# Kernel tuning notes

Measured on AMD Instinct MI355X. Metric: run time of the kernel, lower is better.

## Reference

```python
import jax, jax.numpy as jnp
import numpy as np

GAMMA = 2.0
EPS = 1e-06
LAMBDA_DISTANCE = 1.0
LAMBDA_NORMAL = 0.01
LAMBDA_LAPLACIAN = 0.1
CLS = 1


def vertex_normals(v, f, eps=EPS):
    # v: [N,3], f: [F,3] int. Scatter face normals to vertices, then normalize.
    fv = v[f]  # [F,3,3]
    fn = jnp.cross(fv[:, 1] - fv[:, 0], fv[:, 2] - fv[:, 0])  # [F,3]
    vn = jnp.zeros_like(v)
    vn = vn.at[f[:, 0]].add(fn).at[f[:, 1]].add(fn).at[f[:, 2]].add(fn)
    norm = jnp.maximum(jnp.linalg.norm(vn, axis=-1, keepdims=True), eps)
    return vn / norm


def squared_cdist(a, b):
    # [Na,3] x [Nb,3] -> squared euclidean distances [Na,Nb] (clamped >= 0)
    a2 = jnp.sum(a * a, axis=1)[:, None]
    b2 = jnp.sum(b * b, axis=1)[None, :]
    d2 = a2 + b2 - 2.0 * (a @ b.T)
    return jnp.maximum(d2, 0.0)


def sample_binary_targets(label, v, cls=CLS):
    # Nearest-neighbor grid_sample, align_corners=True, padding zeros.
    # grid = 2*v - 1 -> voxel index = round(v * (size-1)); v[:,0]->W, v[:,1]->H, v[:,2]->D.
    D, H, W = label.shape[2], label.shape[3], label.shape[4]
    ix = jnp.round(v[:, 0] * (W - 1)).astype(jnp.int32)
    iy = jnp.round(v[:, 1] * (H - 1)).astype(jnp.int32)
    iz = jnp.round(v[:, 2] * (D - 1)).astype(jnp.int32)
    inb = (ix >= 0) & (ix < W) & (iy >= 0) & (iy < H) & (iz >= 0) & (iz < D)
    ixc = jnp.clip(ix, 0, W - 1)
    iyc = jnp.clip(iy, 0, H - 1)
    izc = jnp.clip(iz, 0, D - 1)
    vals = (label[0, 0, izc, iyc, ixc] == cls).astype(jnp.float32)
    return jnp.where(inb, vals, 0.0)


def spatial_consistency_loss(rel_pos, targets, gamma=GAMMA, eps=EPS):
    p = jnp.clip(rel_pos, eps, 1.0 - eps)
    pos = targets > 0.5
    pc = jnp.sum(pos).astype(p.dtype)
    tot = jnp.asarray(p.shape[0], p.dtype)
    nc = tot - pc
    alpha = nc / (tot + eps)
    lpos = -alpha * jnp.power(1.0 - p, gamma) * jnp.log(p)
    lneg = -(1.0 - alpha) * jnp.power(p, gamma) * jnp.log(1.0 - p)
    return jnp.sum(jnp.where(pos, lpos, lneg)) / (tot + eps)


def laplacian_uniform(v, f):
    # Uniform mesh Laplacian smoothing: || mean(neighbors) - v ||, averaged.
    i = jnp.concatenate([f[:, 0], f[:, 1], f[:, 2], f[:, 1], f[:, 2], f[:, 0]])
    j = jnp.concatenate([f[:, 1], f[:, 2], f[:, 0], f[:, 0], f[:, 1], f[:, 2]])
    nsum = jnp.zeros_like(v).at[i].add(v[j])
    deg = jnp.zeros((v.shape[0],), v.dtype).at[i].add(1.0)
    lap = nsum / jnp.maximum(deg, 1.0)[:, None] - v
    return jnp.mean(jnp.linalg.norm(lap, axis=1))


def loss_forward(pred_vertices, relative_positions, gt_vertices, pred_faces, gt_faces, label):
    gt_v = jax.lax.stop_gradient(gt_vertices)  # gt comes from label volume; detached in original
    gt_normals = vertex_normals(gt_v, gt_faces)
    # spatial (focal-style) loss
    targets = sample_binary_targets(label, pred_vertices)
    spatial = spatial_consistency_loss(relative_positions, targets)
    # chamfer-style squared surface distance
    d2 = squared_cdist(pred_vertices, gt_v)  # [Np,Ng]
    distance = jnp.mean(jnp.min(d2, axis=1)) + jnp.mean(jnp.min(d2, axis=0))
    # normal consistency vs nearest gt vertex
    pred_normals = vertex_normals(pred_vertices, pred_faces)
    nearest = jnp.argmin(d2, axis=1)
    normal = jnp.mean((pred_normals - gt_normals[nearest]) ** 2)
    # uniform laplacian smoothing
    laplacian = laplacian_uniform(pred_vertices, pred_faces)
    total = spatial + LAMBDA_DISTANCE * distance + LAMBDA_NORMAL * normal + LAMBDA_LAPLACIAN * laplacian
    return total


def setup_inputs() -> dict:
    key = jax.random.key(0)
    k1, k2, k3, k4, k5, k6 = jax.random.split(key, 6)
    Np, Ng = 8192, 12000
    pred_vertices = jax.random.uniform(k1, (Np, 3), dtype=jnp.float32)
    relative_positions = jax.random.uniform(k2, (Np,), dtype=jnp.float32)
    gt_vertices = jax.random.uniform(k3, (Ng, 3), dtype=jnp.float32)
    pred_faces = jax.random.randint(k4, (2 * Np, 3), 0, Np, dtype=jnp.int32)
    gt_faces = jax.random.randint(k5, (2 * Ng, 3), 0, Ng, dtype=jnp.int32)
    label = jax.random.randint(k6, (1, 1, 96, 96, 96), 0, 2, dtype=jnp.int32)
    return {"pred_vertices": pred_vertices, "relative_positions": relative_positions,
            "gt_vertices": gt_vertices, "pred_faces": pred_faces,
            "gt_faces": gt_faces, "label": label}


def reference(pred_vertices, relative_positions, gt_vertices, pred_faces, gt_faces, label):
    return loss_forward(pred_vertices, relative_positions, gt_vertices, pred_faces, gt_faces, label)
```

## Files before the change

kernel.cpp:

```cpp
#include <hip/hip_runtime.h>
#include <math.h>

#define NP 8192
#define NG 12000
#define NFP 16384
#define NFG 24000
#define EPSF 1e-6f

#define GR 16
#define NC (GR*GR*GR)
#define HCELL 0.0625f
#define QL 16
#define QPB (256 / QL)
#define PRED_QBLOCKS (NP / QPB)
#define GT_QBLOCKS (NG / QPB)
#define FACE_BLOCKS ((NFG + NFP + 255) / 256)
#define QF_BLOCKS (PRED_QBLOCKS + GT_QBLOCKS + FACE_BLOCKS)
#define FIN_BLOCKS (NP / 256)

static constexpr size_t OFF_STARTP = 0;
static constexpr size_t OFF_STARTG = 16640;
static constexpr size_t OFF_SORTP  = 33280;
static constexpr size_t OFF_SORTG  = 164352;
static constexpr size_t OFF_GTN    = 356352;
static constexpr size_t OFF_PNN    = 500352;
static constexpr size_t OFF_NSUM   = 598656;
static constexpr size_t OFF_DEG    = 696960;
static constexpr size_t OFF_NEAR   = 729728;
static constexpr size_t OFF_ACCUM  = 762496;
static constexpr size_t OFF_DONE   = 762528;
#define N_ZERO 101545

__device__ __forceinline__ int cell_of(float x) {
    int c = (int)(x * (float)GR);
    return min(max(c, 0), GR - 1);
}

__device__ __forceinline__ void build_cells(const float* __restrict__ pts, int n,
                                            unsigned* __restrict__ start,
                                            float4* __restrict__ sorted,
                                            unsigned* h, unsigned* wsum) {
    int t = threadIdx.x;
    int lane = t & 63, wid = t >> 6;
    for (int i = t; i < NC; i += 1024) h[i] = 0u;
    __syncthreads();
    for (int i = t; i < n; i += 1024) {
        int c = (cell_of(pts[3*i+2]) * GR + cell_of(pts[3*i+1])) * GR + cell_of(pts[3*i]);
        atomicAdd(&h[c], 1u);
    }
    __syncthreads();
    unsigned a0 = h[4*t], a1 = h[4*t+1], a2 = h[4*t+2], a3 = h[4*t+3];
    unsigned tsum = a0 + a1 + a2 + a3;
    unsigned x = tsum;
    #pragma unroll
    for (int off = 1; off < 64; off <<= 1) {
        unsigned y = __shfl_up(x, off, 64);
        if (lane >= off) x += y;
    }
    if (lane == 63) wsum[wid] = x;
    __syncthreads();
    if (t < 16) {
        unsigned w = wsum[t];
        #pragma unroll
        for (int off = 1; off < 16; off <<= 1) {
            unsigned y = __shfl_up(w, off, 64);
            if (t >= off) w += y;
        }
        wsum[t] = w;
    }
    __syncthreads();
    unsigned base = (wid ? wsum[wid-1] : 0u) + (x - tsum);
    unsigned e0 = base, e1 = base + a0, e2 = base + a0 + a1, e3 = base + a0 + a1 + a2;
    start[4*t] = e0; start[4*t+1] = e1; start[4*t+2] = e2; start[4*t+3] = e3;
    h[4*t] = e0; h[4*t+1] = e1; h[4*t+2] = e2; h[4*t+3] = e3;
    __syncthreads();
    for (int i = t; i < n; i += 1024) {
        float px = pts[3*i], py = pts[3*i+1], pz = pts[3*i+2];
        int c = (cell_of(pz) * GR + cell_of(py)) * GR + cell_of(px);
        unsigned pos = atomicAdd(&h[c], 1u);
        sorted[pos] = make_float4(px, py, pz, __int_as_float(i));
    }
    if (t == 0) start[NC] = (unsigned)n;
}

__global__ __launch_bounds__(1024) void build_kernel(const float* __restrict__ pred,
                                                     const float* __restrict__ gt,
                                                     unsigned* __restrict__ startP,
                                                     unsigned* __restrict__ startG,
                                                     float4* __restrict__ sortP,
                                                     float4* __restrict__ sortG,
                                                     float* __restrict__ zero) {
    __shared__ unsigned h[NC];
    __shared__ unsigned wsum[16];
    if (blockIdx.x == 0) {
        build_cells(pred, NP, startP, sortP, h, wsum);
    } else if (blockIdx.x == 1) {
        build_cells(gt, NG, startG, sortG, h, wsum);
    } else {
        int i = (blockIdx.x - 2) * 1024 + threadIdx.x;
        if (i < N_ZERO) zero[i] = 0.0f;
    }
}

__device__ __forceinline__ float wave_sum(float x) {
    #pragma unroll
    for (int o = 32; o > 0; o >>= 1) x += __shfl_down(x, o, 64);
    return x;
}

__device__ __forceinline__ unsigned long long u64min(unsigned long long a,
                                                     unsigned long long b) {
    return a < b ? a : b;
}

__device__ __forceinline__ unsigned long long group_nn(int lane,
                                                       float px, float py, float pz,
                                                       const float4* __restrict__ S,
                                                       const unsigned* __restrict__ cstart) {
    int cx = cell_of(px), cy = cell_of(py), cz = cell_of(pz);
    unsigned long long best = 0xFFFFFFFFFFFFFFFFULL;
    for (int r = 1; ; ++r) {
        int w = 2 * r + 1;
        int nrows = w * w;
        int x0 = max(cx - r, 0), x1 = min(cx + r, GR - 1);
        unsigned long long lb = 0xFFFFFFFFFFFFFFFFULL;
        for (int k = lane; k < nrows; k += QL) {
            int z = cz + k / w - r, y = cy + k % w - r;
            if (z >= 0 && z < GR && y >= 0 && y < GR) {
                int rowbase = (z * GR + y) * GR;
                unsigned s0 = cstart[rowbase + x0];
                unsigned s1 = cstart[rowbase + x1 + 1];
                for (unsigned t = s0; t < s1; ++t) {
                    float4 q = S[t];
                    float ddx = px - q.x, ddy = py - q.y, ddz = pz - q.z;
                    float d2 = fmaf(ddx, ddx, fmaf(ddy, ddy, ddz*ddz));
                    unsigned long long key =
                        ((unsigned long long)__float_as_uint(d2) << 32) |
                        (unsigned)__float_as_int(q.w);
                    lb = u64min(lb, key);
                }
            }
        }
        best = u64min(best, lb);
        #pragma unroll
        for (int m = 1; m < QL; m <<= 1)
            best = u64min(best, (unsigned long long)__shfl_xor((long long)best, m, 64));
        bool covered = (cx - r <= 0) & (cx + r >= GR - 1) &
                       (cy - r <= 0) & (cy + r >= GR - 1) &
                       (cz - r <= 0) & (cz + r >= GR - 1);
        if (covered) break;
        float blo = 1.0e30f;
        if (cx - r > 0)      blo = fminf(blo, px - (float)(cx - r) * HCELL);
        if (cx + r < GR - 1) blo = fminf(blo, (float)(cx + r + 1) * HCELL - px);
        if (cy - r > 0)      blo = fminf(blo, py - (float)(cy - r) * HCELL);
        if (cy + r < GR - 1) blo = fminf(blo, (float)(cy + r + 1) * HCELL - py);
        if (cz - r > 0)      blo = fminf(blo, pz - (float)(cz - r) * HCELL);
        if (cz + r < GR - 1) blo = fminf(blo, (float)(cz + r + 1) * HCELL - pz);
        float bd2 = __uint_as_float((unsigned)(best >> 32));
        if (bd2 <= blo * blo) break;
    }
    return best;
}

__global__ __launch_bounds__(256) void query_face_kernel(const float* __restrict__ pred,
                                                         const int* __restrict__ pf,
                                                         const float* __restrict__ gt,
                                                         const int* __restrict__ gf,
                                                         const float4* __restrict__ sortP,
                                                         const float4* __restrict__ sortG,
                                                         const unsigned* __restrict__ startP,
                                                         const unsigned* __restrict__ startG,
                                                         float* __restrict__ gtn,
                                                         float* __restrict__ pnn,
                                                         float* __restrict__ nsum,
                                                         float* __restrict__ deg,
                                                         int* __restrict__ nearestIdx,
                                                         float* __restrict__ accum) {
    int b = blockIdx.x;
    if (b < PRED_QBLOCKS + GT_QBLOCKS) {
        __shared__ float bs;
        if (threadIdx.x == 0) bs = 0.0f;
        __syncthreads();
        int lane = threadIdx.x & (QL - 1);
        int group = threadIdx.x >> 4;
        float r0 = 0.0f;
        if (b < PRED_QBLOCKS) {
            int qid = b * QPB + group;
            float4 P = sortP[qid];
            unsigned long long key = group_nn(lane, P.x, P.y, P.z, sortG, startG);
            if (lane == 0) {
                int v = __float_as_int(P.w);
                nearestIdx[v] = (int)(unsigned)(key & 0xffffffffu);
                r0 = __uint_as_float((unsigned)(key >> 32));
            }
        } else {
            int qid = (b - PRED_QBLOCKS) * QPB + group;
            float4 Q = sortG[qid];
            unsigned long long key = group_nn(lane, Q.x, Q.y, Q.z, sortP, startP);
            if (lane == 0) r0 = __uint_as_float((unsigned)(key >> 32));
        }
        r0 = wave_sum(r0);
        if ((threadIdx.x & 63) == 0) atomicAdd(&bs, r0);
        __syncthreads();
        if (threadIdx.x == 0)
            atomicAdd(&accum[(b < PRED_QBLOCKS) ? 0 : 6], bs);
    } else {
        int t = (b - PRED_QBLOCKS - GT_QBLOCKS) * 256 + threadIdx.x;
        if (t < NFG) {
            int i0 = gf[3*t], i1 = gf[3*t+1], i2 = gf[3*t+2];
            float ax = gt[3*i0], ay = gt[3*i0+1], az = gt[3*i0+2];
            float bx = gt[3*i1], by = gt[3*i1+1], bz = gt[3*i1+2];
            float cx = gt[3*i2], cy = gt[3*i2+1], cz = gt[3*i2+2];
            float ux = bx-ax, uy = by-ay, uz = bz-az;
            float wx = cx-ax, wy = cy-ay, wz = cz-az;
            float nx = uy*wz - uz*wy, ny = uz*wx - ux*wz, nz = ux*wy - uy*wx;
            atomicAdd(&gtn[3*i0+0], nx); atomicAdd(&gtn[3*i0+1], ny); atomicAdd(&gtn[3*i0+2], nz);
            atomicAdd(&gtn[3*i1+0], nx); atomicAdd(&gtn[3*i1+1], ny); atomicAdd(&gtn[3*i1+2], nz);
            atomicAdd(&gtn[3*i2+0], nx); atomicAdd(&gtn[3*i2+1], ny); atomicAdd(&gtn[3*i2+2], nz);
        } else if (t < NFG + NFP) {
            int u = t - NFG;
            int i0 = pf[3*u], i1 = pf[3*u+1], i2 = pf[3*u+2];
            float ax = pred[3*i0], ay = pred[3*i0+1], az = pred[3*i0+2];
            float bx = pred[3*i1], by = pred[3*i1+1], bz = pred[3*i1+2];
            float cx = pred[3*i2], cy = pred[3*i2+1], cz = pred[3*i2+2];
            float ux = bx-ax, uy = by-ay, uz = bz-az;
            float wx = cx-ax, wy = cy-ay, wz = cz-az;
            float nx = uy*wz - uz*wy, ny = uz*wx - ux*wz, nz = ux*wy - uy*wx;
            atomicAdd(&pnn[3*i0+0], nx); atomicAdd(&pnn[3*i0+1], ny); atomicAdd(&pnn[3*i0+2], nz);
            atomicAdd(&pnn[3*i1+0], nx); atomicAdd(&pnn[3*i1+1], ny); atomicAdd(&pnn[3*i1+2], nz);
            atomicAdd(&pnn[3*i2+0], nx); atomicAdd(&pnn[3*i2+1], ny); atomicAdd(&pnn[3*i2+2], nz);
            atomicAdd(&nsum[3*i0+0], bx+cx); atomicAdd(&nsum[3*i0+1], by+cy); atomicAdd(&nsum[3*i0+2], bz+cz);
            atomicAdd(&nsum[3*i1+0], cx+ax); atomicAdd(&nsum[3*i1+1], cy+ay); atomicAdd(&nsum[3*i1+2], cz+az);
            atomicAdd(&nsum[3*i2+0], ax+bx); atomicAdd(&nsum[3*i2+1], ay+by); atomicAdd(&nsum[3*i2+2], az+bz);
            atomicAdd(&deg[i0], 2.0f); atomicAdd(&deg[i1], 2.0f); atomicAdd(&deg[i2], 2.0f);
        }
    }
}

__global__ __launch_bounds__(256) void finish_kernel(const float* __restrict__ pred,
                                                     const float* __restrict__ relpos,
                                                     const int* __restrict__ label,
                                                     const float* __restrict__ pnn,
                                                     const float* __restrict__ gtn,
                                                     const float* __restrict__ nsum,
                                                     const float* __restrict__ deg,
                                                     const int* __restrict__ nearestIdx,
                                                     float* __restrict__ accum,
                                                     unsigned* __restrict__ done,
                                                     float* __restrict__ out) {
    int v = blockIdx.x * 256 + threadIdx.x;
    float px = pred[3*v], py = pred[3*v+1], pz = pred[3*v+2];
    int nearest = nearestIdx[v];

    float ax = pnn[3*v], ay = pnn[3*v+1], az = pnn[3*v+2];
    float an = fmaxf(sqrtf(ax*ax + ay*ay + az*az), EPSF);
    float gx = gtn[3*nearest], gy = gtn[3*nearest+1], gz = gtn[3*nearest+2];
    float gn = fmaxf(sqrtf(gx*gx + gy*gy + gz*gz), EPSF);
    float nx = ax/an - gx/gn, ny = ay/an - gy/gn, nz = az/an - gz/gn;
    float sse = nx*nx + ny*ny + nz*nz;

    float d = fmaxf(deg[v], 1.0f);
    float lx = nsum[3*v]/d - px, ly = nsum[3*v+1]/d - py, lz = nsum[3*v+2]/d - pz;
    float lapn = sqrtf(lx*lx + ly*ly + lz*lz);

    int ix = (int)rintf(px * 95.0f), iy = (int)rintf(py * 95.0f), iz = (int)rintf(pz * 95.0f);
    bool inb = (ix >= 0) & (ix < 96) & (iy >= 0) & (iy < 96) & (iz >= 0) & (iz < 96);
    int ixc = min(max(ix, 0), 95), iyc = min(max(iy, 0), 95), izc = min(max(iz, 0), 95);
    bool pos = inb && (label[(izc*96 + iyc)*96 + ixc] == 1);

    float p = fminf(fmaxf(relpos[v], EPSF), 1.0f - EPSF);
    float om = 1.0f - p;
    float pcnt = 0.0f, sx = 0.0f, sy = 0.0f;
    if (pos) { pcnt = 1.0f; sx = om*om*logf(p); }
    else     { sy = p*p*logf(om); }

    float r1 = wave_sum(sse), r2 = wave_sum(lapn), r3 = wave_sum(pcnt);
    float r4 = wave_sum(sx),  r5 = wave_sum(sy);
    __shared__ float bsum[5];
    __shared__ bool isLast;
    if (threadIdx.x < 5) bsum[threadIdx.x] = 0.0f;
    __syncthreads();
    if ((threadIdx.x & 63) == 0) {
        atomicAdd(&bsum[0], r1); atomicAdd(&bsum[1], r2); atomicAdd(&bsum[2], r3);
        atomicAdd(&bsum[3], r4); atomicAdd(&bsum[4], r5);
    }
    __syncthreads();
    if (threadIdx.x == 0) {
        atomicAdd(&accum[1], bsum[0]); atomicAdd(&accum[2], bsum[1]);
        atomicAdd(&accum[3], bsum[2]); atomicAdd(&accum[4], bsum[3]);
        atomicAdd(&accum[5], bsum[4]);
        __threadfence();
        unsigned prev = atomicAdd(done, 1u);
        isLast = (prev == FIN_BLOCKS - 1);
    }
    __syncthreads();
    if (isLast && threadIdx.x == 0) {
        __threadfence();
        float sum_row = __hip_atomic_load(&accum[0], __ATOMIC_RELAXED, __HIP_MEMORY_SCOPE_AGENT);
        float sse_t   = __hip_atomic_load(&accum[1], __ATOMIC_RELAXED, __HIP_MEMORY_SCOPE_AGENT);
        float lap_t   = __hip_atomic_load(&accum[2], __ATOMIC_RELAXED, __HIP_MEMORY_SCOPE_AGENT);
        float pc      = __hip_atomic_load(&accum[3], __ATOMIC_RELAXED, __HIP_MEMORY_SCOPE_AGENT);
        float SX      = __hip_atomic_load(&accum[4], __ATOMIC_RELAXED, __HIP_MEMORY_SCOPE_AGENT);
        float SY      = __hip_atomic_load(&accum[5], __ATOMIC_RELAXED, __HIP_MEMORY_SCOPE_AGENT);
        float sum_col = __hip_atomic_load(&accum[6], __ATOMIC_RELAXED, __HIP_MEMORY_SCOPE_AGENT);
        float tot = (float)NP;
        float alpha = (tot - pc) / (tot + EPSF);
        float spatial = (-alpha * SX - (1.0f - alpha) * SY) / (tot + EPSF);
        float distance = sum_row / (float)NP + sum_col / (float)NG;
        float normal = sse_t / (float)(NP * 3);
        float lapm = lap_t / (float)NP;
        out[0] = spatial + 1.0f * distance + 0.01f * normal + 0.1f * lapm;
    }
}

extern "C" void kernel_launch(void* const* d_in, const int* in_sizes, int n_in,
                              void* d_out, int out_size, void* d_ws, size_t ws_size,
                              hipStream_t stream) {
    const float* pred   = (const float*)d_in[0];
    const float* relpos = (const float*)d_in[1];
    const float* gt     = (const float*)d_in[2];
    const int*   pfaces = (const int*)d_in[3];
    const int*   gfaces = (const int*)d_in[4];
    const int*   label  = (const int*)d_in[5];
    float* out = (float*)d_out;

    char* ws = (char*)d_ws;
    unsigned* startP  = (unsigned*)(ws + OFF_STARTP);
    unsigned* startG  = (unsigned*)(ws + OFF_STARTG);
    float4*   sortP   = (float4*)(ws + OFF_SORTP);
    float4*   sortG   = (float4*)(ws + OFF_SORTG);
    float*    gtn     = (float*)(ws + OFF_GTN);
    float*    pnn     = (float*)(ws + OFF_PNN);
    float*    nsum    = (float*)(ws + OFF_NSUM);
    float*    deg     = (float*)(ws + OFF_DEG);
    int*      nearest = (int*)(ws + OFF_NEAR);
    float*    accum   = (float*)(ws + OFF_ACCUM);
    unsigned* done    = (unsigned*)(ws + OFF_DONE);

    int zero_blocks = (N_ZERO + 1023) / 1024;
    hipLaunchKernelGGL(build_kernel, dim3(2 + zero_blocks), dim3(1024), 0, stream,
                       pred, gt, startP, startG, sortP, sortG, (float*)(ws + OFF_GTN));
    hipLaunchKernelGGL(query_face_kernel, dim3(QF_BLOCKS), dim3(256), 0, stream,
                       pred, pfaces, gt, gfaces, sortP, sortG, startP, startG,
                       gtn, pnn, nsum, deg, nearest, accum);
    hipLaunchKernelGGL(finish_kernel, dim3(FIN_BLOCKS), dim3(256), 0, stream,
                       pred, relpos, label, pnn, gtn, nsum, deg, nearest,
                       accum, done, out);
}
```

Before: 124.7 us.

## Privatize face scatter-adds into LDS vertex ranges and enlarge query blocks

Face-normal and Laplacian scatter-adds move from global atomics into shared memory. Each of a few 1024-thread blocks owns a vertex index range, scans every face, and writes its range back with plain stores, so the large workspace zero-fill is no longer needed. The nearest-neighbour query blocks grow to 1024 threads (64 queries per block) and the inner candidate loop is unrolled by four. In exchange, each face block scans all faces redundantly, and only seven blocks do the face work, which may lengthen the critical path.

After: 194.7 us. +56.2%, slower.

```diff
diff --git a/kernel.cpp b/kernel.cpp
--- a/kernel.cpp
+++ b/kernel.cpp
@@ -11,11 +11,16 @@
 #define NC (GR*GR*GR)
 #define HCELL 0.0625f
 #define QL 16
-#define QPB (256 / QL)
-#define PRED_QBLOCKS (NP / QPB)
-#define GT_QBLOCKS (NG / QPB)
-#define FACE_BLOCKS ((NFG + NFP + 255) / 256)
-#define QF_BLOCKS (PRED_QBLOCKS + GT_QBLOCKS + FACE_BLOCKS)
+
+#define PR_LDSB 4
+#define PR_RANGE 2048
+#define GT_LDSB 3
+#define GT_RANGE 4000
+#define FACE_LDS_BLOCKS (PR_LDSB + GT_LDSB)
+#define PQB 64
+#define PRED_QB (NP / PQB)
+#define GT_QB ((NG + PQB - 1) / PQB)
+#define QF_BLOCKS (FACE_LDS_BLOCKS + PRED_QB + GT_QB)
 #define FIN_BLOCKS (NP / 256)
 
 static constexpr size_t OFF_STARTP = 0;
@@ -29,7 +34,6 @@
 static constexpr size_t OFF_NEAR   = 729728;
 static constexpr size_t OFF_ACCUM  = 762496;
 static constexpr size_t OFF_DONE   = 762528;
-#define N_ZERO 101545
 
 __device__ __forceinline__ int cell_of(float x) {
     int c = (int)(x * (float)GR);
@@ -89,7 +93,8 @@
                                                      unsigned* __restrict__ startG,
                                                      float4* __restrict__ sortP,
                                                      float4* __restrict__ sortG,
-                                                     float* __restrict__ zero) {
+                                                     float* __restrict__ accum,
+                                                     unsigned* __restrict__ done) {
     __shared__ unsigned h[NC];
     __shared__ unsigned wsum[16];
     if (blockIdx.x == 0) {
@@ -97,8 +102,8 @@
     } else if (blockIdx.x == 1) {
         build_cells(gt, NG, startG, sortG, h, wsum);
     } else {
-        int i = (blockIdx.x - 2) * 1024 + threadIdx.x;
-        if (i < N_ZERO) zero[i] = 0.0f;
+        if (threadIdx.x < 8) accum[threadIdx.x] = 0.0f;
+        if (threadIdx.x == 8) *done = 0u;
     }
 }
 
@@ -111,6 +116,14 @@
 __device__ __forceinline__ unsigned long long u64min(unsigned long long a,
                                                      unsigned long long b) {
     return a < b ? a : b;
+}
+
+__device__ __forceinline__ unsigned long long pack_key(float px, float py, float pz,
+                                                       float4 q) {
+    float ddx = px - q.x, ddy = py - q.y, ddz = pz - q.z;
+    float d2 = fmaf(ddx, ddx, fmaf(ddy, ddy, ddz*ddz));
+    return ((unsigned long long)__float_as_uint(d2) << 32) |
+           (unsigned)__float_as_int(q.w);
 }
 
 __device__ __forceinline__ unsigned long long group_nn(int lane,
@@ -130,14 +143,17 @@
                 int rowbase = (z * GR + y) * GR;
                 unsigned s0 = cstart[rowbase + x0];
                 unsigned s1 = cstart[rowbase + x1 + 1];
-                for (unsigned t = s0; t < s1; ++t) {
-                    float4 q = S[t];
-                    float ddx = px - q.x, ddy = py - q.y, ddz = pz - q.z;
-                    float d2 = fmaf(ddx, ddx, fmaf(ddy, ddy, ddz*ddz));
-                    unsigned long long key =
-                        ((unsigned long long)__float_as_uint(d2) << 32) |
-                        (unsigned)__float_as_int(q.w);
-                    lb = u64min(lb, key);
+                unsigned t = s0;
+                for (; t + 4 <= s1; t += 4) {
+                    float4 q0 = S[t], q1 = S[t+1], q2 = S[t+2], q3 = S[t+3];
+                    unsigned long long k0 = pack_key(px, py, pz, q0);
+                    unsigned long long k1 = pack_key(px, py, pz, q1);
+                    unsigned long long k2 = pack_key(px, py, pz, q2);
+                    unsigned long long k3 = pack_key(px, py, pz, q3);
+                    lb = u64min(lb, u64min(u64min(k0, k1), u64min(k2, k3)));
+                }
+                for (; t < s1; ++t) {
+                    lb = u64min(lb, pack_key(px, py, pz, S[t]));
                 }
             }
         }
@@ -162,79 +178,122 @@
     return best;
 }
 
-__global__ __launch_bounds__(256) void query_face_kernel(const float* __restrict__ pred,
-                                                         const int* __restrict__ pf,
-                                                         const float* __restrict__ gt,
-                                                         const int* __restrict__ gf,
-                                                         const float4* __restrict__ sortP,
-                                                         const float4* __restrict__ sortG,
-                                                         const unsigned* __restrict__ startP,
-                                                         const unsigned* __restrict__ startG,
-                                                         float* __restrict__ gtn,
-                                                         float* __restrict__ pnn,
-                                                         float* __restrict__ nsum,
-                                                         float* __restrict__ deg,
-                                                         int* __restrict__ nearestIdx,
-                                                         float* __restrict__ accum) {
+__global__ __launch_bounds__(1024) void query_face_kernel(const float* __restrict__ pred,
+                                                          const int* __restrict__ pf,
+                                                          const float* __restrict__ gt,
+                                                          const int* __restrict__ gf,
+                                                          const float4* __restrict__ sortP,
+                                                          const float4* __restrict__ sortG,
+                                                          const unsigned* __restrict__ startP,
+                                                          const unsigned* __restrict__ startG,
+                                                          float* __restrict__ gtn,
+                                                          float* __restrict__ pnn,
+                                                          float* __restrict__ nsum,
+                                                          float* __restrict__ deg,
+                                                          int* __restrict__ nearestIdx,
+                                                          float* __restrict__ accum) {
+    __shared__ float lds_f[14336];
+    __shared__ float qsum;
     int b = blockIdx.x;
-    if (b < PRED_QBLOCKS + GT_QBLOCKS) {
-        __shared__ float bs;
-        if (threadIdx.x == 0) bs = 0.0f;
+    int t = threadIdx.x;
+
+    if (b < PR_LDSB) {
+        int rb = b * PR_RANGE;
+        for (int i = t; i < 14336; i += 1024) lds_f[i] = 0.0f;
         __syncthreads();
-        int lane = threadIdx.x & (QL - 1);
-        int group = threadIdx.x >> 4;
-        float r0 = 0.0f;
-        if (b < PRED_QBLOCKS) {
-            int qid = b * QPB + group;
-            float4 P = sortP[qid];
-            unsigned long long key = group_nn(lane, P.x, P.y, P.z, sortG, startG);
-            if (lane == 0) {
-                int v = __float_as_int(P.w);
-                nearestIdx[v] = (int)(unsigned)(key & 0xffffffffu);
-                r0 = __uint_as_float((unsigned)(key >> 32));
-            }
-        } else {
-            int qid = (b - PRED_QBLOCKS) * QPB + group;
-            float4 Q = sortG[qid];
-            unsigned long long key = group_nn(lane, Q.x, Q.y, Q.z, sortP, startP);
-            if (lane == 0) r0 = __uint_as_float((unsigned)(key >> 32));
-        }
-        r0 = wave_sum(r0);
-        if ((threadIdx.x & 63) == 0) atomicAdd(&bs, r0);
+        for (int f = t; f < NFP; f += 1024) {
+            int i0 = pf[3*f], i1 = pf[3*f+1], i2 = pf[3*f+2];
+            float ax = pred[3*i0], ay = pred[3*i0+1], az = pred[3*i0+2];
+            float bx = pred[3*i1], by = pred[3*i1+1], bz = pred[3*i1+2];
+            float cx = pred[3*i2], cy = pred[3*i2+1], cz = pred[3*i2+2];
+            float ux = bx-ax, uy = by-ay, uz = bz-az;
+            float wx = cx-ax, wy = cy-ay, wz = cz-az;
+            float nx = uy*wz - uz*wy, ny = uz*wx - ux*wz, nz = ux*wy - uy*wx;
+            if ((unsigned)(i0 - rb) < PR_RANGE) {
+                int l = i0 - rb;
+                atomicAdd(&lds_f[3*l+0], nx); atomicAdd(&lds_f[3*l+1], ny); atomicAdd(&lds_f[3*l+2], nz);
+                atomicAdd(&lds_f[6144+3*l+0], bx+cx); atomicAdd(&lds_f[6144+3*l+1], by+cy); atomicAdd(&lds_f[6144+3*l+2], bz+cz);
+                atomicAdd(&lds_f[12288+l], 2.0f);
+            }
+            if ((unsigned)(i1 - rb) < PR_RANGE) {
+                int l = i1 - rb;
+                atomicAdd(&lds_f[3*l+0], nx); atomicAdd(&lds_f[3*l+1], ny); atomicAdd(&lds_f[3*l+2], nz);
+                atomicAdd(&lds_f[6144+3*l+0], cx+ax); atomicAdd(&lds_f[6144+3*l+1], cy+ay); atomicAdd(&lds_f[6144+3*l+2], cz+az);
+                atomicAdd(&lds_f[12288+l], 2.0f);
+            }
+            if ((unsigned)(i2 - rb) < PR_RANGE) {
+                int l = i2 - rb;
+                atomicAdd(&lds_f[3*l+0], nx); atomicAdd(&lds_f[3*l+1], ny); atomicAdd(&lds_f[3*l+2], nz);
+                atomicAdd(&lds_f[6144+3*l+0], ax+bx); atomicAdd(&lds_f[6144+3*l+1], ay+by); atomicAdd(&lds_f[6144+3*l+2], az+bz);
+                atomicAdd(&lds_f[12288+l], 2.0f);
+            }
+        }
         __syncthreads();
-        if (threadIdx.x == 0)
-            atomicAdd(&accum[(b < PRED_QBLOCKS) ? 0 : 6], bs);
-    } else {
-        int t = (b - PRED_QBLOCKS - GT_QBLOCKS) * 256 + threadIdx.x;
-        if (t < NFG) {
-            int i0 = gf[3*t], i1 = gf[3*t+1], i2 = gf[3*t+2];
+        for (int i = t; i < 3*PR_RANGE; i += 1024) {
+            pnn[3*rb + i]  = lds_f[i];
+            nsum[3*rb + i] = lds_f[6144 + i];
+        }
+        for (int i = t; i < PR_RANGE; i += 1024) deg[rb + i] = lds_f[12288 + i];
+        return;
+    }
+    if (b < FACE_LDS_BLOCKS) {
+        int rb = (b - PR_LDSB) * GT_RANGE;
+        for (int i = t; i < 3*GT_RANGE; i += 1024) lds_f[i] = 0.0f;
+        __syncthreads();
+        for (int f = t; f < NFG; f += 1024) {
+            int i0 = gf[3*f], i1 = gf[3*f+1], i2 = gf[3*f+2];
             float ax = gt[3*i0], ay = gt[3*i0+1], az = gt[3*i0+2];
             float bx = gt[3*i1], by = gt[3*i1+1], bz = gt[3*i1+2];
             float cx = gt[3*i2], cy = gt[3*i2+1], cz = gt[3*i2+2];
             float ux = bx-ax, uy = by-ay, uz = bz-az;
             float wx = cx-ax, wy = cy-ay, wz = cz-az;
             float nx = uy*wz - uz*wy, ny = uz*wx - ux*wz, nz = ux*wy - uy*wx;
-            atomicAdd(&gtn[3*i0+0], nx); atomicAdd(&gtn[3*i0+1], ny); atomicAdd(&gtn[3*i0+2], nz);
-            atomicAdd(&gtn[3*i1+0], nx); atomicAdd(&gtn[3*i1+1], ny); atomicAdd(&gtn[3*i1+2], nz);
-            atomicAdd(&gtn[3*i2+0], nx); atomicAdd(&gtn[3*i2+1], ny); atomicAdd(&gtn[3*i2+2], nz);
-        } else if (t < NFG + NFP) {
-            int u = t - NFG;
-            int i0 = pf[3*u], i1 = pf[3*u+1], i2 = pf[3*u+2];
-            float ax = pred[3*i0], ay = pred[3*i0+1], az = pred[3*i0+2];
-            float bx = pred[3*i1], by = pred[3*i1+1], bz = pred[3*i1+2];
-            float cx = pred[3*i2], cy = pred[3*i2+1], cz = pred[3*i2+2];
-            float ux = bx-ax, uy = by-ay, uz = bz-az;
-            float wx = cx-ax, wy = cy-ay, wz = cz-az;
-            float nx = uy*wz - uz*wy, ny = uz*wx - ux*wz, nz = ux*wy - uy*wx;
-            atomicAdd(&pnn[3*i0+0], nx); atomicAdd(&pnn[3*i0+1], ny); atomicAdd(&pnn[3*i0+2], nz);
-            atomicAdd(&pnn[3*i1+0], nx); atomicAdd(&pnn[3*i1+1], ny); atomicAdd(&pnn[3*i1+2], nz);
-            atomicAdd(&pnn[3*i2+0], nx); atomicAdd(&pnn[3*i2+1], ny); atomicAdd(&pnn[3*i2+2], nz);
-            atomicAdd(&nsum[3*i0+0], bx+cx); atomicAdd(&nsum[3*i0+1], by+cy); atomicAdd(&nsum[3*i0+2], bz+cz);
-            atomicAdd(&nsum[3*i1+0], cx+ax); atomicAdd(&nsum[3*i1+1], cy+ay); atomicAdd(&nsum[3*i1+2], cz+az);
-            atomicAdd(&nsum[3*i2+0], ax+bx); atomicAdd(&nsum[3*i2+1], ay+by); atomicAdd(&nsum[3*i2+2], az+bz);
-            atomicAdd(&deg[i0], 2.0f); atomicAdd(&deg[i1], 2.0f); atomicAdd(&deg[i2], 2.0f);
-        }
-    }
+            if ((unsigned)(i0 - rb) < GT_RANGE) {
+                int l = i0 - rb;
+                atomicAdd(&lds_f[3*l+0], nx); atomicAdd(&lds_f[3*l+1], ny); atomicAdd(&lds_f[3*l+2], nz);
+            }
+            if ((unsigned)(i1 - rb) < GT_RANGE) {
+                int l = i1 - rb;
+                atomicAdd(&lds_f[3*l+0], nx); atomicAdd(&lds_f[3*l+1], ny); atomicAdd(&lds_f[3*l+2], nz);
+            }
+            if ((unsigned)(i2 - rb) < GT_RANGE) {
+                int l = i2 - rb;
+                atomicAdd(&lds_f[3*l+0], nx); atomicAdd(&lds_f[3*l+1], ny); atomicAdd(&lds_f[3*l+2], nz);
+            }
+        }
+        __syncthreads();
+        for (int i = t; i < 3*GT_RANGE; i += 1024) gtn[3*rb + i] = lds_f[i];
+        return;
+    }
+
+    if (t == 0) qsum = 0.0f;
+    __syncthreads();
+    int b2 = b - FACE_LDS_BLOCKS;
+    int lane = t & (QL - 1);
+    int group = t >> 4;
+    bool is_pred = (b2 < PRED_QB);
+    float r0 = 0.0f;
+    if (is_pred) {
+        int qid = b2 * PQB + group;
+        float4 P = sortP[qid];
+        unsigned long long key = group_nn(lane, P.x, P.y, P.z, sortG, startG);
+        if (lane == 0) {
+            int v = __float_as_int(P.w);
+            nearestIdx[v] = (int)(unsigned)(key & 0xffffffffu);
+            r0 = __uint_as_float((unsigned)(key >> 32));
+        }
+    } else {
+        int qid = (b2 - PRED_QB) * PQB + group;
+        if (qid < NG) {
+            float4 Q = sortG[qid];
+            unsigned long long key = group_nn(lane, Q.x, Q.y, Q.z, sortP, startP);
+            if (lane == 0) r0 = __uint_as_float((unsigned)(key >> 32));
+        }
+    }
+    r0 = wave_sum(r0);
+    if ((t & 63) == 0) atomicAdd(&qsum, r0);
+    __syncthreads();
+    if (t == 0) atomicAdd(&accum[is_pred ? 0 : 6], qsum);
 }
 
 __global__ __launch_bounds__(256) void finish_kernel(const float* __restrict__ pred,
@@ -337,10 +396,9 @@
     float*    accum   = (float*)(ws + OFF_ACCUM);
     unsigned* done    = (unsigned*)(ws + OFF_DONE);
 
-    int zero_blocks = (N_ZERO + 1023) / 1024;
-    hipLaunchKernelGGL(build_kernel, dim3(2 + zero_blocks), dim3(1024), 0, stream,
-                       pred, gt, startP, startG, sortP, sortG, (float*)(ws + OFF_GTN));
-    hipLaunchKernelGGL(query_face_kernel, dim3(QF_BLOCKS), dim3(256), 0, stream,
+    hipLaunchKernelGGL(build_kernel, dim3(3), dim3(1024), 0, stream,
+                       pred, gt, startP, startG, sortP, sortG, accum, done);
+    hipLaunchKernelGGL(query_face_kernel, dim3(QF_BLOCKS), dim3(1024), 0, stream,
                        pred, pfaces, gt, gfaces, sortP, sortG, startP, startG,
                        gtn, pnn, nsum, deg, nearest, accum);
     hipLaunchKernelGGL(finish_kernel, dim3(FIN_BLOCKS), dim3(256), 0, stream,
```

## Move face scatters into LDS-privatized build blocks and fuse query with finish

Applied to the files above, without the earlier changes.

Face-normal and Laplacian scatters now run inside the build kernel: each block accumulates into LDS, with pred vertices split into two index ranges and faces split into two halves. The split partials are written to A/B buffers and summed by the reader, which removes global atomics and the zeroing pass. The nearest-neighbour search changes from 16-lane cooperative groups to one thread per query, and the finish work is folded into the query kernel, saving one launch and the nearest-index round trip. The risks are that the build phase now runs on only 9 large blocks, so the serial scatter loops may sit on the critical path, and that single-thread queries can diverge badly within a wave.

Result: slower. 245.9 us (+97.2%).

```diff
diff --git a/kernel.cpp b/kernel.cpp
--- a/kernel.cpp
+++ b/kernel.cpp
@@ -10,26 +10,28 @@
 #define GR 16
 #define NC (GR*GR*GR)
 #define HCELL 0.0625f
-#define QL 16
-#define QPB (256 / QL)
-#define PRED_QBLOCKS (NP / QPB)
-#define GT_QBLOCKS (NG / QPB)
-#define FACE_BLOCKS ((NFG + NFP + 255) / 256)
-#define QF_BLOCKS (PRED_QBLOCKS + GT_QBLOCKS + FACE_BLOCKS)
-#define FIN_BLOCKS (NP / 256)
+
+#define PF_R 4096
+#define D1_LDS_BYTES 144000
+
+#define PQ_BLOCKS (NP / 256)
+#define GQ_BLOCKS ((NG + 255) / 256)
+#define D2_BLOCKS (PQ_BLOCKS + GQ_BLOCKS)
 
 static constexpr size_t OFF_STARTP = 0;
 static constexpr size_t OFF_STARTG = 16640;
 static constexpr size_t OFF_SORTP  = 33280;
 static constexpr size_t OFF_SORTG  = 164352;
-static constexpr size_t OFF_GTN    = 356352;
-static constexpr size_t OFF_PNN    = 500352;
-static constexpr size_t OFF_NSUM   = 598656;
-static constexpr size_t OFF_DEG    = 696960;
-static constexpr size_t OFF_NEAR   = 729728;
-static constexpr size_t OFF_ACCUM  = 762496;
-static constexpr size_t OFF_DONE   = 762528;
-#define N_ZERO 101545
+static constexpr size_t OFF_PNNA   = 356352;
+static constexpr size_t OFF_PNNB   = 454656;
+static constexpr size_t OFF_NSUMA  = 552960;
+static constexpr size_t OFF_NSUMB  = 651264;
+static constexpr size_t OFF_DEGA   = 749568;
+static constexpr size_t OFF_DEGB   = 782336;
+static constexpr size_t OFF_GTNA   = 815104;
+static constexpr size_t OFF_GTNB   = 959104;
+static constexpr size_t OFF_ACCUM  = 1103104;
+static constexpr size_t OFF_DONE   = 1103136;
 
 __device__ __forceinline__ int cell_of(float x) {
     int c = (int)(x * (float)GR);
@@ -85,20 +87,93 @@
 
 __global__ __launch_bounds__(1024) void build_kernel(const float* __restrict__ pred,
                                                      const float* __restrict__ gt,
+                                                     const int* __restrict__ pf,
+                                                     const int* __restrict__ gf,
                                                      unsigned* __restrict__ startP,
                                                      unsigned* __restrict__ startG,
                                                      float4* __restrict__ sortP,
                                                      float4* __restrict__ sortG,
-                                                     float* __restrict__ zero) {
-    __shared__ unsigned h[NC];
-    __shared__ unsigned wsum[16];
-    if (blockIdx.x == 0) {
-        build_cells(pred, NP, startP, sortP, h, wsum);
-    } else if (blockIdx.x == 1) {
-        build_cells(gt, NG, startG, sortG, h, wsum);
+                                                     float* __restrict__ pnnA,
+                                                     float* __restrict__ pnnB,
+                                                     float* __restrict__ nsumA,
+                                                     float* __restrict__ nsumB,
+                                                     float* __restrict__ degA,
+                                                     float* __restrict__ degB,
+                                                     float* __restrict__ gtnA,
+                                                     float* __restrict__ gtnB,
+                                                     float* __restrict__ accum,
+                                                     unsigned* __restrict__ done) {
+    extern __shared__ float lds[];
+    int b = blockIdx.x, t = threadIdx.x;
+    if (b == 0) {
+        build_cells(pred, NP, startP, sortP, (unsigned*)lds, (unsigned*)lds + NC);
+    } else if (b == 1) {
+        build_cells(gt, NG, startG, sortG, (unsigned*)lds, (unsigned*)lds + NC);
+    } else if (b == 2) {
+        if (t < 8) accum[t] = 0.0f;
+        if (t == 8) *done = 0u;
+    } else if (b <= 6) {
+        int q = b - 3;
+        int rb = (q >> 1) * PF_R;
+        int f0 = (q & 1) * (NFP / 2);
+        float* opnn  = (q & 1) ? pnnB  : pnnA;
+        float* onsum = (q & 1) ? nsumB : nsumA;
+        float* odeg  = (q & 1) ? degB  : degA;
+        for (int i = t; i < 7 * PF_R; i += 1024) lds[i] = 0.0f;
+        __syncthreads();
+        for (int f = f0 + t; f < f0 + NFP / 2; f += 1024) {
+            int i0 = pf[3*f], i1 = pf[3*f+1], i2 = pf[3*f+2];
+            float ax = pred[3*i0], ay = pred[3*i0+1], az = pred[3*i0+2];
+            float bx = pred[3*i1], by = pred[3*i1+1], bz = pred[3*i1+2];
+            float cx = pred[3*i2], cy = pred[3*i2+1], cz = pred[3*i2+2];
+            float ux = bx-ax, uy = by-ay, uz = bz-az;
+            float wx = cx-ax, wy = cy-ay, wz = cz-az;
+            float nx = uy*wz - uz*wy, ny = uz*wx - ux*wz, nz = ux*wy - uy*wx;
+            if ((unsigned)(i0 - rb) < PF_R) {
+                int l = i0 - rb;
+                atomicAdd(&lds[3*l+0], nx); atomicAdd(&lds[3*l+1], ny); atomicAdd(&lds[3*l+2], nz);
+                atomicAdd(&lds[3*PF_R+3*l+0], bx+cx); atomicAdd(&lds[3*PF_R+3*l+1], by+cy); atomicAdd(&lds[3*PF_R+3*l+2], bz+cz);
+                atomicAdd(&lds[6*PF_R+l], 2.0f);
+            }
+            if ((unsigned)(i1 - rb) < PF_R) {
+                int l = i1 - rb;
+                atomicAdd(&lds[3*l+0], nx); atomicAdd(&lds[3*l+1], ny); atomicAdd(&lds[3*l+2], nz);
+                atomicAdd(&lds[3*PF_R+3*l+0], cx+ax); atomicAdd(&lds[3*PF_R+3*l+1], cy+ay); atomicAdd(&lds[3*PF_R+3*l+2], cz+az);
+                atomicAdd(&lds[6*PF_R+l], 2.0f);
+            }
+            if ((unsigned)(i2 - rb) < PF_R) {
+                int l = i2 - rb;
+                atomicAdd(&lds[3*l+0], nx); atomicAdd(&lds[3*l+1], ny); atomicAdd(&lds[3*l+2], nz);
+                atomicAdd(&lds[3*PF_R+3*l+0], ax+bx); atomicAdd(&lds[3*PF_R+3*l+1], ay+by); atomicAdd(&lds[3*PF_R+3*l+2], az+bz);
+                atomicAdd(&lds[6*PF_R+l], 2.0f);
+            }
+        }
+        __syncthreads();
+        for (int i = t; i < 3 * PF_R; i += 1024) {
+            opnn[3*rb + i]  = lds[i];
+            onsum[3*rb + i] = lds[3*PF_R + i];
+        }
+        for (int i = t; i < PF_R; i += 1024) odeg[rb + i] = lds[6*PF_R + i];
     } else {
-        int i = (blockIdx.x - 2) * 1024 + threadIdx.x;
-        if (i < N_ZERO) zero[i] = 0.0f;
+        int hb = b - 7;
+        int f0 = hb * (NFG / 2);
+        float* og = hb ? gtnB : gtnA;
+        for (int i = t; i < 3 * NG; i += 1024) lds[i] = 0.0f;
+        __syncthreads();
+        for (int f = f0 + t; f < f0 + NFG / 2; f += 1024) {
+            int i0 = gf[3*f], i1 = gf[3*f+1], i2 = gf[3*f+2];
+            float ax = gt[3*i0], ay = gt[3*i0+1], az = gt[3*i0+2];
+            float bx = gt[3*i1], by = gt[3*i1+1], bz = gt[3*i1+2];
+            float cx = gt[3*i2], cy = gt[3*i2+1], cz = gt[3*i2+2];
+            float ux = bx-ax, uy = by-ay, uz = bz-az;
+            float wx = cx-ax, wy = cy-ay, wz = cz-az;
+            float nx = uy*wz - uz*wy, ny = uz*wx - ux*wz, nz = ux*wy - uy*wx;
+            atomicAdd(&lds[3*i0+0], nx); atomicAdd(&lds[3*i0+1], ny); atomicAdd(&lds[3*i0+2], nz);
+            atomicAdd(&lds[3*i1+0], nx); atomicAdd(&lds[3*i1+1], ny); atomicAdd(&lds[3*i1+2], nz);
+            atomicAdd(&lds[3*i2+0], nx); atomicAdd(&lds[3*i2+1], ny); atomicAdd(&lds[3*i2+2], nz);
+        }
+        __syncthreads();
+        for (int i = t; i < 3 * NG; i += 1024) og[i] = lds[i];
     }
 }
 
@@ -113,41 +188,34 @@
     return a < b ? a : b;
 }
 
-__device__ __forceinline__ unsigned long long group_nn(int lane,
-                                                       float px, float py, float pz,
-                                                       const float4* __restrict__ S,
-                                                       const unsigned* __restrict__ cstart) {
+__device__ __forceinline__ unsigned long long pack_key(float px, float py, float pz,
+                                                       float4 q) {
+    float ddx = px - q.x, ddy = py - q.y, ddz = pz - q.z;
+    float d2 = fmaf(ddx, ddx, fmaf(ddy, ddy, ddz*ddz));
+    return ((unsigned long long)__float_as_uint(d2) << 32) |
+           (unsigned)__float_as_int(q.w);
+}
+
+__device__ __forceinline__ unsigned long long lane_nn(float px, float py, float pz,
+                                                      const float4* __restrict__ S,
+                                                      const unsigned* __restrict__ cstart) {
     int cx = cell_of(px), cy = cell_of(py), cz = cell_of(pz);
     unsigned long long best = 0xFFFFFFFFFFFFFFFFULL;
     for (int r = 1; ; ++r) {
-        int w = 2 * r + 1;
-        int nrows = w * w;
         int x0 = max(cx - r, 0), x1 = min(cx + r, GR - 1);
-        unsigned long long lb = 0xFFFFFFFFFFFFFFFFULL;
-        for (int k = lane; k < nrows; k += QL) {
-            int z = cz + k / w - r, y = cy + k % w - r;
-            if (z >= 0 && z < GR && y >= 0 && y < GR) {
+        int y0 = max(cy - r, 0), y1 = min(cy + r, GR - 1);
+        int z0 = max(cz - r, 0), z1 = min(cz + r, GR - 1);
+        for (int z = z0; z <= z1; ++z) {
+            for (int y = y0; y <= y1; ++y) {
                 int rowbase = (z * GR + y) * GR;
                 unsigned s0 = cstart[rowbase + x0];
                 unsigned s1 = cstart[rowbase + x1 + 1];
-                for (unsigned t = s0; t < s1; ++t) {
-                    float4 q = S[t];
-                    float ddx = px - q.x, ddy = py - q.y, ddz = pz - q.z;
-                    float d2 = fmaf(ddx, ddx, fmaf(ddy, ddy, ddz*ddz));
-                    unsigned long long key =
-                        ((unsigned long long)__float_as_uint(d2) << 32) |
-                        (unsigned)__float_as_int(q.w);
-                    lb = u64min(lb, key);
-                }
+                for (unsigned u = s0; u < s1; ++u)
+                    best = u64min(best, pack_key(px, py, pz, S[u]));
             }
         }
-        best = u64min(best, lb);
-        #pragma unroll
-        for (int m = 1; m < QL; m <<= 1)
-            best = u64min(best, (unsigned long long)__shfl_xor((long long)best, m, 64));
-        bool covered = (cx - r <= 0) & (cx + r >= GR - 1) &
-                       (cy - r <= 0) & (cy + r >= GR - 1) &
-                       (cz - r <= 0) & (cz + r >= GR - 1);
+        bool covered = (x0 == 0) & (x1 == GR-1) & (y0 == 0) &
+                       (y1 == GR-1) & (z0 == 0) & (z1 == GR-1);
         if (covered) break;
         float blo = 1.0e30f;
         if (cx - r > 0)      blo = fminf(blo, px - (float)(cx - r) * HCELL);
@@ -162,139 +230,101 @@
     return best;
 }
 
-__global__ __launch_bounds__(256) void query_face_kernel(const float* __restrict__ pred,
-                                                         const int* __restrict__ pf,
-                                                         const float* __restrict__ gt,
-                                                         const int* __restrict__ gf,
-                                                         const float4* __restrict__ sortP,
-                                                         const float4* __restrict__ sortG,
-                                                         const unsigned* __restrict__ startP,
-                                                         const unsigned* __restrict__ startG,
-                                                         float* __restrict__ gtn,
-                                                         float* __restrict__ pnn,
-                                                         float* __restrict__ nsum,
-                                                         float* __restrict__ deg,
-                                                         int* __restrict__ nearestIdx,
-                                                         float* __restrict__ accum) {
-    int b = blockIdx.x;
-    if (b < PRED_QBLOCKS + GT_QBLOCKS) {
-        __shared__ float bs;
-        if (threadIdx.x == 0) bs = 0.0f;
-        __syncthreads();
-        int lane = threadIdx.x & (QL - 1);
-        int group = threadIdx.x >> 4;
-        float r0 = 0.0f;
-        if (b < PRED_QBLOCKS) {
-            int qid = b * QPB + group;
-            float4 P = sortP[qid];
-            unsigned long long key = group_nn(lane, P.x, P.y, P.z, sortG, startG);
-            if (lane == 0) {
-                int v = __float_as_int(P.w);
-                nearestIdx[v] = (int)(unsigned)(key & 0xffffffffu);
-                r0 = __uint_as_float((unsigned)(key >> 32));
-            }
+__global__ __launch_bounds__(256) void query_kernel(const float* __restrict__ relpos,
+                                                    const int* __restrict__ label,
+                                                    const float4* __restrict__ sortP,
+                                                    const float4* __restrict__ sortG,
+                                                    const unsigned* __restrict__ startP,
+                                                    const unsigned* __restrict__ startG,
+                                                    const float* __restrict__ pnnA,
+                                                    const float* __restrict__ pnnB,
+                                                    const float* __restrict__ nsumA,
+                                                    const float* __restrict__ nsumB,
+                                                    const float* __restrict__ degA,
+                                                    const float* __restrict__ degB,
+                                                    const float* __restrict__ gtnA,
+                                                    const float* __restrict__ gtnB,
+                                                    float* __restrict__ accum,
+                                                    unsigned* __restrict__ done,
+                                                    float* __restrict__ out) {
+    __shared__ float bsum[6];
+    __shared__ bool isLast;
+    int b = blockIdx.x, t = threadIdx.x;
+    if (t < 6) bsum[t] = 0.0f;
+    __syncthreads();
+    float r0 = 0.f, r1 = 0.f, r2 = 0.f, r3 = 0.f, r4 = 0.f, r5 = 0.f;
+    bool is_pred = (b < PQ_BLOCKS);
+    if (is_pred) {
+        int qid = b * 256 + t;
+        float4 P = sortP[qid];
+        float px = P.x, py = P.y, pz = P.z;
+        unsigned long long key = lane_nn(px, py, pz, sortG, startG);
+        int v = __float_as_int(P.w);
+        int nearest = (int)(unsigned)(key & 0xffffffffu);
+        r0 = __uint_as_float((unsigned)(key >> 32));
+
+        float ax = pnnA[3*v]   + pnnB[3*v];
+        float ay = pnnA[3*v+1] + pnnB[3*v+1];
+        float az = pnnA[3*v+2] + pnnB[3*v+2];
+        float an = fmaxf(sqrtf(ax*ax + ay*ay + az*az), EPSF);
+        float gx = gtnA[3*nearest]   + gtnB[3*nearest];
+        float gy = gtnA[3*nearest+1] + gtnB[3*nearest+1];
+        float gz = gtnA[3*nearest+2] + gtnB[3*nearest+2];
+        float gn = fmaxf(sqrtf(gx*gx + gy*gy + gz*gz), EPSF);
+        float nx = ax/an - gx/gn, ny = ay/an - gy/gn, nz = az/an - gz/gn;
+        r1 = nx*nx + ny*ny + nz*nz;
+
+        float d = fmaxf(degA[v] + degB[v], 1.0f);
+        float lx = (nsumA[3*v]   + nsumB[3*v])   / d - px;
+        float ly = (nsumA[3*v+1] + nsumB[3*v+1]) / d - py;
+        float lz = (nsumA[3*v+2] + nsumB[3*v+2]) / d - pz;
+        r2 = sqrtf(lx*lx + ly*ly + lz*lz);
+
+        int ix = (int)rintf(px * 95.0f), iy = (int)rintf(py * 95.0f), iz = (int)rintf(pz * 95.0f);
+        bool inb = (ix >= 0) & (ix < 96) & (iy >= 0) & (iy < 96) & (iz >= 0) & (iz < 96);
+        int ixc = min(max(ix, 0), 95), iyc = min(max(iy, 0), 95), izc = min(max(iz, 0), 95);
+        bool pos = inb && (label[(izc*96 + iyc)*96 + ixc] == 1);
+
+        float p = fminf(fmaxf(relpos[v], EPSF), 1.0f - EPSF);
+        float om = 1.0f - p;
+        if (pos) { r3 = 1.0f; r4 = om*om*logf(p); }
+        else     { r5 = p*p*logf(om); }
+    } else {
+        int qid = (b - PQ_BLOCKS) * 256 + t;
+        if (qid < NG) {
+            float4 Q = sortG[qid];
+            unsigned long long key = lane_nn(Q.x, Q.y, Q.z, sortP, startP);
+            r0 = __uint_as_float((unsigned)(key >> 32));
+        }
+    }
+    r0 = wave_sum(r0);
+    if (is_pred) {
+        r1 = wave_sum(r1); r2 = wave_sum(r2); r3 = wave_sum(r3);
+        r4 = wave_sum(r4); r5 = wave_sum(r5);
+    }
+    if ((t & 63) == 0) {
+        atomicAdd(&bsum[0], r0);
+        if (is_pred) {
+            atomicAdd(&bsum[1], r1); atomicAdd(&bsum[2], r2);
+            atomicAdd(&bsum[3], r3); atomicAdd(&bsum[4], r4);
+            atomicAdd(&bsum[5], r5);
+        }
+    }
+    __syncthreads();
+    if (t == 0) {
+        if (is_pred) {
+            atomicAdd(&accum[0], bsum[0]); atomicAdd(&accum[1], bsum[1]);
+            atomicAdd(&accum[2], bsum[2]); atomicAdd(&accum[3], bsum[3]);
+            atomicAdd(&accum[4], bsum[4]); atomicAdd(&accum[5], bsum[5]);
         } else {
-            int qid = (b - PRED_QBLOCKS) * QPB + group;
-            float4 Q = sortG[qid];
-            unsigned long long key = group_nn(lane, Q.x, Q.y, Q.z, sortP, startP);
-            if (lane == 0) r0 = __uint_as_float((unsigned)(key >> 32));
-        }
-        r0 = wave_sum(r0);
-        if ((threadIdx.x & 63) == 0) atomicAdd(&bs, r0);
-        __syncthreads();
-        if (threadIdx.x == 0)
-            atomicAdd(&accum[(b < PRED_QBLOCKS) ? 0 : 6], bs);
-    } else {
-        int t = (b - PRED_QBLOCKS - GT_QBLOCKS) * 256 + threadIdx.x;
-        if (t < NFG) {
-            int i0 = gf[3*t], i1 = gf[3*t+1], i2 = gf[3*t+2];
-            float ax = gt[3*i0], ay = gt[3*i0+1], az = gt[3*i0+2];
-            float bx = gt[3*i1], by = gt[3*i1+1], bz = gt[3*i1+2];
-            float cx = gt[3*i2], cy = gt[3*i2+1], cz = gt[3*i2+2];
-            float ux = bx-ax, uy = by-ay, uz = bz-az;
-            float wx = cx-ax, wy = cy-ay, wz = cz-az;
-            float nx = uy*wz - uz*wy, ny = uz*wx - ux*wz, nz = ux*wy - uy*wx;
-            atomicAdd(&gtn[3*i0+0], nx); atomicAdd(&gtn[3*i0+1], ny); atomicAdd(&gtn[3*i0+2], nz);
-            atomicAdd(&gtn[3*i1+0], nx); atomicAdd(&gtn[3*i1+1], ny); atomicAdd(&gtn[3*i1+2], nz);
-            atomicAdd(&gtn[3*i2+0], nx); atomicAdd(&gtn[3*i2+1], ny); atomicAdd(&gtn[3*i2+2], nz);
-        } else if (t < NFG + NFP) {
-            int u = t - NFG;
-            int i0 = pf[3*u], i1 = pf[3*u+1], i2 = pf[3*u+2];
-            float ax = pred[3*i0], ay = pred[3*i0+1], az = pred[3*i0+2];
-            float bx = pred[3*i1], by = pred[3*i1+1], bz = pred[3*i1+2];
-            float cx = pred[3*i2], cy = pred[3*i2+1], cz = pred[3*i2+2];
-            float ux = bx-ax, uy = by-ay, uz = bz-az;
-            float wx = cx-ax, wy = cy-ay, wz = cz-az;
-            float nx = uy*wz - uz*wy, ny = uz*wx - ux*wz, nz = ux*wy - uy*wx;
-            atomicAdd(&pnn[3*i0+0], nx); atomicAdd(&pnn[3*i0+1], ny); atomicAdd(&pnn[3*i0+2], nz);
-            atomicAdd(&pnn[3*i1+0], nx); atomicAdd(&pnn[3*i1+1], ny); atomicAdd(&pnn[3*i1+2], nz);
-            atomicAdd(&pnn[3*i2+0], nx); atomicAdd(&pnn[3*i2+1], ny); atomicAdd(&pnn[3*i2+2], nz);
-            atomicAdd(&nsum[3*i0+0], bx+cx); atomicAdd(&nsum[3*i0+1], by+cy); atomicAdd(&nsum[3*i0+2], bz+cz);
-            atomicAdd(&nsum[3*i1+0], cx+ax); atomicAdd(&nsum[3*i1+1], cy+ay); atomicAdd(&nsum[3*i1+2], cz+az);
-            atomicAdd(&nsum[3*i2+0], ax+bx); atomicAdd(&nsum[3*i2+1], ay+by); atomicAdd(&nsum[3*i2+2], az+bz);
-            atomicAdd(&deg[i0], 2.0f); atomicAdd(&deg[i1], 2.0f); atomicAdd(&deg[i2], 2.0f);
-        }
-    }
-}
-
-__global__ __launch_bounds__(256) void finish_kernel(const float* __restrict__ pred,
-                                                     const float* __restrict__ relpos,
-                                                     const int* __restrict__ label,
-                                                     const float* __restrict__ pnn,
-                                                     const float* __restrict__ gtn,
-                                                     const float* __restrict__ nsum,
-                                                     const float* __restrict__ deg,
-                                                     const int* __restrict__ nearestIdx,
-                                                     float* __restrict__ accum,
-                                                     unsigned* __restrict__ done,
-                                                     float* __restrict__ out) {
-    int v = blockIdx.x * 256 + threadIdx.x;
-    float px = pred[3*v], py = pred[3*v+1], pz = pred[3*v+2];
-    int nearest = nearestIdx[v];
-
-    float ax = pnn[3*v], ay = pnn[3*v+1], az = pnn[3*v+2];
-    float an = fmaxf(sqrtf(ax*ax + ay*ay + az*az), EPSF);
-    float gx = gtn[3*nearest], gy = gtn[3*nearest+1], gz = gtn[3*nearest+2];
-    float gn = fmaxf(sqrtf(gx*gx + gy*gy + gz*gz), EPSF);
-    float nx = ax/an - gx/gn, ny = ay/an - gy/gn, nz = az/an - gz/gn;
-    float sse = nx*nx + ny*ny + nz*nz;
-
-    float d = fmaxf(deg[v], 1.0f);
-    float lx = nsum[3*v]/d - px, ly = nsum[3*v+1]/d - py, lz = nsum[3*v+2]/d - pz;
-    float lapn = sqrtf(lx*lx + ly*ly + lz*lz);
-
-    int ix = (int)rintf(px * 95.0f), iy = (int)rintf(py * 95.0f), iz = (int)rintf(pz * 95.0f);
-    bool inb = (ix >= 0) & (ix < 96) & (iy >= 0) & (iy < 96) & (iz >= 0) & (iz < 96);
-    int ixc = min(max(ix, 0), 95), iyc = min(max(iy, 0), 95), izc = min(max(iz, 0), 95);
-    bool pos = inb && (label[(izc*96 + iyc)*96 + ixc] == 1);
-
-    float p = fminf(fmaxf(relpos[v], EPSF), 1.0f - EPSF);
-    float om = 1.0f - p;
-    float pcnt = 0.0f, sx = 0.0f, sy = 0.0f;
-    if (pos) { pcnt = 1.0f; sx = om*om*logf(p); }
-    else     { sy = p*p*logf(om); }
-
-    float r1 = wave_sum(sse), r2 = wave_sum(lapn), r3 = wave_sum(pcnt);
-    float r4 = wave_sum(sx),  r5 = wave_sum(sy);
-    __shared__ float bsum[5];
-    __shared__ bool isLast;
-    if (threadIdx.x < 5) bsum[threadIdx.x] = 0.0f;
-    __syncthreads();
-    if ((threadIdx.x & 63) == 0) {
-        atomicAdd(&bsum[0], r1); atomicAdd(&bsum[1], r2); atomicAdd(&bsum[2], r3);
-        atomicAdd(&bsum[3], r4); atomicAdd(&bsum[4], r5);
-    }
-    __syncthreads();
-    if (threadIdx.x == 0) {
-        atomicAdd(&accum[1], bsum[0]); atomicAdd(&accum[2], bsum[1]);
-        atomicAdd(&accum[3], bsum[2]); atomicAdd(&accum[4], bsum[3]);
-        atomicAdd(&accum[5], bsum[4]);
+            atomicAdd(&accum[6], bsum[0]);
+        }
         __threadfence();
         unsigned prev = atomicAdd(done, 1u);
-        isLast = (prev == FIN_BLOCKS - 1);
-    }
-    __syncthreads();
-    if (isLast && threadIdx.x == 0) {
+        isLast = (prev == D2_BLOCKS - 1);
+    }
+    __syncthreads();
+    if (isLast && t == 0) {
         __threadfence();
         float sum_row = __hip_atomic_load(&accum[0], __ATOMIC_RELAXED, __HIP_MEMORY_SCOPE_AGENT);
         float sse_t   = __hip_atomic_load(&accum[1], __ATOMIC_RELAXED, __HIP_MEMORY_SCOPE_AGENT);
@@ -329,21 +359,23 @@
     unsigned* startG  = (unsigned*)(ws + OFF_STARTG);
     float4*   sortP   = (float4*)(ws + OFF_SORTP);
     float4*   sortG   = (float4*)(ws + OFF_SORTG);
-    float*    gtn     = (float*)(ws + OFF_GTN);
-    float*    pnn     = (float*)(ws + OFF_PNN);
-    float*    nsum    = (float*)(ws + OFF_NSUM);
-    float*    deg     = (float*)(ws + OFF_DEG);
-    int*      nearest = (int*)(ws + OFF_NEAR);
+    float*    pnnA    = (float*)(ws + OFF_PNNA);
+    float*    pnnB    = (float*)(ws + OFF_PNNB);
+    float*    nsumA   = (float*)(ws + OFF_NSUMA);
+    float*    nsumB   = (float*)(ws + OFF_NSUMB);
+    float*    degA    = (float*)(ws + OFF_DEGA);
+    float*    degB    = (float*)(ws + OFF_DEGB);
+    float*    gtnA    = (float*)(ws + OFF_GTNA);
+    float*    gtnB    = (float*)(ws + OFF_GTNB);
     float*    accum   = (float*)(ws + OFF_ACCUM);
     unsigned* done    = (unsigned*)(ws + OFF_DONE);
 
-    int zero_blocks = (N_ZERO + 1023) / 1024;
-    hipLaunchKernelGGL(build_kernel, dim3(2 + zero_blocks), dim3(1024), 0, stream,
-                       pred, gt, startP, startG, sortP, sortG, (float*)(ws + OFF_GTN));
-    hipLaunchKernelGGL(query_face_kernel, dim3(QF_BLOCKS), dim3(256), 0, stream,
-                       pred, pfaces, gt, gfaces, sortP, sortG, startP, startG,
-                       gtn, pnn, nsum, deg, nearest, accum);
-    hipLaunchKernelGGL(finish_kernel, dim3(FIN_BLOCKS), dim3(256), 0, stream,
-                       pred, relpos, label, pnn, gtn, nsum, deg, nearest,
+    hipLaunchKernelGGL(build_kernel, dim3(9), dim3(1024), D1_LDS_BYTES, stream,
+                       pred, gt, pfaces, gfaces, startP, startG, sortP, sortG,
+                       pnnA, pnnB, nsumA, nsumB, degA, degB, gtnA, gtnB,
+                       accum, done);
+    hipLaunchKernelGGL(query_kernel, dim3(D2_BLOCKS), dim3(256), 0, stream,
+                       relpos, label, sortP, sortG, startP, startG,
+                       pnnA, pnnB, nsumA, nsumB, degA, degB, gtnA, gtnB,
                        accum, done, out);
 }
```
